# Optimization experiments

Hardware: AMD Instinct MI355X
Metric: run time of the kernel (lower is better)

## Reference

```python
import jax, jax.numpy as jnp
import numpy as np

EMBED = 1024
HEADS = 16
HEAD_SIZE = EMBED // HEADS


def setup_inputs() -> dict:
    key = jax.random.key(0)
    ks = jax.random.split(key, 12)
    B, S = 2, 2048
    s = 1.0 / np.sqrt(EMBED)
    return {
        "querys": jax.random.normal(ks[0], (B, S, EMBED), jnp.float32),
        "keys": jax.random.normal(ks[1], (B, S, EMBED), jnp.float32),
        "values": jax.random.normal(ks[2], (B, S, EMBED), jnp.float32),
        "Wq": jax.random.normal(ks[3], (EMBED, EMBED), jnp.float32) * s,
        "bq": jax.random.normal(ks[4], (EMBED,), jnp.float32) * s,
        "Wk": jax.random.normal(ks[5], (EMBED, EMBED), jnp.float32) * s,
        "bk": jax.random.normal(ks[6], (EMBED,), jnp.float32) * s,
        "Wv": jax.random.normal(ks[7], (EMBED, EMBED), jnp.float32) * s,
        "bv": jax.random.normal(ks[8], (EMBED,), jnp.float32) * s,
        "Wo": jax.random.normal(ks[9], (EMBED, EMBED), jnp.float32) * s,
        "bo": jax.random.normal(ks[10], (EMBED,), jnp.float32) * s,
    }


def reference(querys, keys, values, Wq, bq, Wk, bk, Wv, bv, Wo, bo):
    B, S, E = querys.shape
    H, D = HEADS, HEAD_SIZE
    # torch nn.Linear: y = x @ W.T + b
    q = (querys @ Wq.T + bq).reshape(B, S, H, D).transpose(0, 2, 1, 3)  # [B,H,S,D]
    k = (keys @ Wk.T + bk).reshape(B, S, H, D).transpose(0, 2, 1, 3)
    v = (values @ Wv.T + bv).reshape(B, S, H, D).transpose(0, 2, 1, 3)
    # NOTE: original scales by head_size**0.05 (faithful to source, likely a bug)
    scale = D ** 0.05
    energy = jnp.einsum("bhqd,bhkd->bhqk", q, k) / scale  # [B,H,S,S]
    attention = jax.nn.softmax(energy, axis=-1)
    out = jnp.einsum("bhqk,bhkd->bhqd", attention, v)  # [B,H,S,D]
    out = out.transpose(0, 2, 1, 3).reshape(B, S, E)
    return out @ Wo.T + bo
```

## Files before the change

kernel.cpp:

```cpp
#include <hip/hip_runtime.h>

typedef __attribute__((ext_vector_type(4))) float f32x4;
typedef __attribute__((ext_vector_type(8))) float f32x8;
typedef __attribute__((ext_vector_type(8))) unsigned short ushort8;
typedef __attribute__((ext_vector_type(4))) unsigned short ushort4v;
typedef __attribute__((ext_vector_type(8))) __bf16 bf16x8;

#define QSCALE 1.17183256f

#if __has_builtin(__builtin_amdgcn_exp2f)
#define EXP2(x) __builtin_amdgcn_exp2f(x)
#else
#define EXP2(x) exp2f(x)
#endif

__device__ __forceinline__ unsigned short f2bf(float x) {
  unsigned u = __float_as_uint(x);
  u += 0x7FFFu + ((u >> 16) & 1u);
  return (unsigned short)(u >> 16);
}

__device__ __forceinline__ ushort8 cvt8(const float* src) {
  float4 x0 = *(const float4*)src;
  float4 x1 = *(const float4*)(src + 4);
  ushort8 v;
  v[0] = f2bf(x0.x); v[1] = f2bf(x0.y); v[2] = f2bf(x0.z); v[3] = f2bf(x0.w);
  v[4] = f2bf(x1.x); v[5] = f2bf(x1.y); v[6] = f2bf(x1.z); v[7] = f2bf(x1.w);
  return v;
}

__device__ __forceinline__ f32x4 mfma16(ushort8 a, ushort8 b, f32x4 c) {
  return __builtin_amdgcn_mfma_f32_16x16x32_bf16(
      __builtin_bit_cast(bf16x8, a), __builtin_bit_cast(bf16x8, b), c, 0, 0, 0);
}
__device__ __forceinline__ f32x4 mfma16b(bf16x8 a, ushort8 b, f32x4 c) {
  return __builtin_amdgcn_mfma_f32_16x16x32_bf16(
      a, __builtin_bit_cast(bf16x8, b), c, 0, 0, 0);
}

__device__ __forceinline__ void gload_lds16(const void* g, void* l) {
  __builtin_amdgcn_global_load_lds(
      (const __attribute__((address_space(1))) void*)g,
      (__attribute__((address_space(3))) void*)l, 16, 0, 0);
}

__global__ __launch_bounds__(256) void cvt_f32_bf16(
    const float* __restrict__ s0, const float* __restrict__ s1, const float* __restrict__ s2,
    const float* __restrict__ s3, const float* __restrict__ s4, const float* __restrict__ s5,
    const float* __restrict__ s6, unsigned short* __restrict__ dstA,
    unsigned short* __restrict__ dstW)
{
  const int z = blockIdx.y;
  const float* src;
  unsigned short* dst;
  int n;
  if (z < 3) {
    src = (z == 0) ? s0 : (z == 1) ? s1 : s2;
    dst = dstA + (size_t)z * 4194304;
    n = 4194304;
  } else {
    src = (z == 3) ? s3 : (z == 4) ? s4 : (z == 5) ? s5 : s6;
    dst = dstW + (size_t)(z - 3) * 1048576;
    n = 1048576;
  }
  int i = (blockIdx.x * 256 + threadIdx.x) * 8;
  const int stride = gridDim.x * 256 * 8;
  for (; i < n; i += stride) *(ushort8*)(dst + i) = cvt8(src + i);
}

__global__ __launch_bounds__(256) void gemm_qkv_bf(
    const unsigned short* __restrict__ Abf, const unsigned short* __restrict__ Wbf,
    const float* __restrict__ bq, const float* __restrict__ bk, const float* __restrict__ bv,
    unsigned short* __restrict__ Qb, unsigned short* __restrict__ Kb,
    unsigned short* __restrict__ Vtb)
{
  __shared__ __align__(16) unsigned short Sl[4][4096];
  const int lin = blockIdx.x + 8 * blockIdx.y + 256 * blockIdx.z;
  const int swz = (lin & 7) * 96 + (lin >> 3);
  const int bx = swz & 7, by = (swz >> 3) & 31, z = swz >> 8;

  const unsigned short* Ap = Abf + (size_t)z * 4194304;
  const unsigned short* Wp = Wbf + (size_t)z * 1048576;
  const float* bp = (z == 0) ? bq : (z == 1) ? bk : bv;

  const int t = threadIdx.x, l = t & 63, w = t >> 6;
  const int lr = l & 15, g = l >> 4;
  const int wm = (w >> 1) * 64, wn = (w & 1) * 64;

  int prow[2], pcol[2];
#pragma unroll
  for (int j = 0; j < 2; ++j) {
    int p = j * 256 + w * 64 + l;
    prow[j] = p >> 2;
    pcol[j] = (p & 3) ^ ((prow[j] >> 1) & 3);
  }

  char* lds0 = (char*)&Sl[0][0];
  const int arow0 = wm + lr, brow0 = wn + lr;
  const int abyte = (arow0 * 32 + (g ^ ((arow0 >> 1) & 3)) * 8) * 2;
  const int bbyte = 8192 + (brow0 * 32 + (g ^ ((brow0 >> 1) & 3)) * 8) * 2;

  f32x4 acc[4][4] = {};

#define STAGE_QKV(bufoff, k0)                                                     \
  {                                                                               \
    _Pragma("unroll") for (int j = 0; j < 2; ++j) {                               \
      gload_lds16(Ap + (size_t)(by * 128 + prow[j]) * 1024 + (k0) + pcol[j] * 8,  \
                  lds0 + (bufoff) + (j * 256 + w * 64) * 16);                     \
      gload_lds16(Wp + (size_t)(bx * 128 + prow[j]) * 1024 + (k0) + pcol[j] * 8,  \
                  lds0 + (bufoff) + 8192 + (j * 256 + w * 64) * 16);              \
    }                                                                             \
  }

  STAGE_QKV(0, 0)
  __syncthreads();

  for (int kt = 0; kt < 32; ++kt) {
    const int curoff = (kt & 1) << 14;
    if (kt < 31) STAGE_QKV(curoff ^ 16384, (kt + 1) * 32)
    const char* pa = lds0 + curoff;
    ushort8 a[4], b[4];
#pragma unroll
    for (int m = 0; m < 4; ++m)
      a[m] = *(const ushort8*)(pa + abyte + m * 1024);
#pragma unroll
    for (int n = 0; n < 4; ++n)
      b[n] = *(const ushort8*)(pa + bbyte + n * 1024);
#pragma unroll
    for (int m = 0; m < 4; ++m)
#pragma unroll
      for (int n = 0; n < 4; ++n)
        acc[m][n] = mfma16(a[m], b[n], acc[m][n]);
    __syncthreads();
  }

  float bias_n[4];
#pragma unroll
  for (int n = 0; n < 4; ++n) bias_n[n] = bp[bx * 128 + wn + n * 16 + lr];

  if (z < 2) {
    const float sc = (z == 0) ? QSCALE : 1.0f;
    unsigned short* Cp = z ? Kb : Qb;
#pragma unroll
    for (int m = 0; m < 4; ++m)
#pragma unroll
      for (int n = 0; n < 4; ++n)
#pragma unroll
        for (int r = 0; r < 4; ++r) {
          float v = (acc[m][n][r] + bias_n[n]) * sc;
          int gm = by * 128 + wm + m * 16 + g * 4 + r;
          int gn = bx * 128 + wn + n * 16 + lr;
          int bb = gm >> 11, s = gm & 2047;
          int h = gn >> 6, d = gn & 63;
          Cp[((size_t)((bb * 16 + h) * 2048 + s) << 6) + d] = f2bf(v);
        }
  } else {
#pragma unroll
    for (int m = 0; m < 4; ++m) {
      int gm0 = by * 128 + wm + m * 16 + g * 4;
      int bb = gm0 >> 11, s0 = gm0 & 2047;
#pragma unroll
      for (int n = 0; n < 4; ++n) {
        int gn = bx * 128 + wn + n * 16 + lr;
        int h = gn >> 6, d = gn & 63;
        ushort4v pk;
#pragma unroll
        for (int r = 0; r < 4; ++r) pk[r] = f2bf(acc[m][n][r] + bias_n[n]);
        *(ushort4v*)&Vtb[((size_t)((bb * 16 + h) * 64 + d) << 11) + s0] = pk;
      }
    }
  }
}

__global__ __launch_bounds__(256) void gemm_o_bf(
    const unsigned short* __restrict__ AO, const unsigned short* __restrict__ Wp,
    const float* __restrict__ bo, float* __restrict__ C)
{
  __shared__ __align__(16) unsigned short Al[2][128 * 32];
  __shared__ __align__(16) unsigned short Wl[2][64 * 32];
  const int lin = blockIdx.x + 16 * blockIdx.y;
  const int swz = (lin & 7) * 64 + (lin >> 3);
  const int bx = swz & 15, by = swz >> 4;

  const int t = threadIdx.x, l = t & 63, w = t >> 6;
  const int lr = l & 15, g = l >> 4;
  const int wm = w * 32;

  int prow[2], pcol[2];
#pragma unroll
  for (int j = 0; j < 2; ++j) {
    int p = j * 256 + w * 64 + l;
    prow[j] = p >> 2;
    pcol[j] = (p & 3) ^ ((prow[j] >> 1) & 3);
  }

  f32x4 acc[2][4] = {};

#define STAGE_O(buf, k0)                                                          \
  {                                                                               \
    _Pragma("unroll") for (int j = 0; j < 2; ++j) {                               \
      gload_lds16(AO + (size_t)(by * 128 + prow[j]) * 1024 + (k0) + pcol[j] * 8,  \
                  &Al[buf][(j * 256 + w * 64) * 8]);                              \
    }                                                                             \
    gload_lds16(Wp + (size_t)(bx * 64 + prow[0]) * 1024 + (k0) + pcol[0] * 8,     \
                &Wl[buf][(w * 64) * 8]);                                          \
  }

  STAGE_O(0, 0)
  __syncthreads();

  for (int kt = 0; kt < 32; ++kt) {
    const int cur = kt & 1;
    if (kt < 31) STAGE_O(cur ^ 1, (kt + 1) * 32)
    ushort8 a[2], b[4];
#pragma unroll
    for (int m = 0; m < 2; ++m) {
      int r = wm + m * 16 + lr;
      a[m] = *(const ushort8*)&Al[cur][r * 32 + (g ^ ((r >> 1) & 3)) * 8];
    }
#pragma unroll
    for (int n = 0; n < 4; ++n) {
      int r = n * 16 + lr;
      b[n] = *(const ushort8*)&Wl[cur][r * 32 + (g ^ ((r >> 1) & 3)) * 8];
    }
#pragma unroll
    for (int m = 0; m < 2; ++m)
#pragma unroll
      for (int n = 0; n < 4; ++n)
        acc[m][n] = mfma16(a[m], b[n], acc[m][n]);
    __syncthreads();
  }

  float bias_n[4];
#pragma unroll
  for (int n = 0; n < 4; ++n) bias_n[n] = bo[bx * 64 + n * 16 + lr];

#pragma unroll
  for (int m = 0; m < 2; ++m)
#pragma unroll
    for (int n = 0; n < 4; ++n)
#pragma unroll
      for (int r = 0; r < 4; ++r) {
        int gm = by * 128 + wm + m * 16 + g * 4 + r;
        int gn = bx * 64 + n * 16 + lr;
        C[(size_t)gm * 1024 + gn] = acc[m][n][r] + bias_n[n];
      }
}

__global__ __launch_bounds__(512) void attn_fwd(
    const unsigned short* __restrict__ Qb, const unsigned short* __restrict__ Kb,
    const unsigned short* __restrict__ Vtb, unsigned short* __restrict__ AO)
{
  __shared__ __align__(16) unsigned short Kl[4][64 * 64];
  __shared__ __align__(16) unsigned short Vl[4][64 * 64];
  const int t = threadIdx.x;
  const int l = t & 63, w = t >> 6;
  const int lr = l & 15, g = l >> 4;
  const int wq = w & 3, kh = w >> 2;
  const int lin = blockIdx.x + 16 * blockIdx.y;
  const int swz = (lin & 7) * 64 + (lin >> 3);
  const int qt = swz & 15, bh = swz >> 4;

  const unsigned short* Qh = Qb + (size_t)bh * (2048 * 64);
  const unsigned short* Kh = Kb + (size_t)bh * (2048 * 64);
  const unsigned short* Vth = Vtb + (size_t)bh * (64 * 2048);

  ushort8 aq[2][2];
#pragma unroll
  for (int m = 0; m < 2; ++m)
#pragma unroll
    for (int kk = 0; kk < 2; ++kk) {
      int q = qt * 128 + wq * 32 + m * 16 + lr;
      aq[m][kk] = *(const ushort8*)&Qh[q * 64 + kk * 32 + g * 8];
    }

  ushort8 ones;
#pragma unroll
  for (int j = 0; j < 8; ++j) ones[j] = 0x3F80;

  f32x4 o[2][4] = {};
  f32x4 lacc[2] = {};

  const int sr = t >> 3, sc = t & 7;
  ushort8 rk, rv;

#define STAGE_ATTN(buf)                                                      \
  {                                                                          \
    *(ushort8*)&Kl[buf][sr * 64 + ((sc ^ (sr & 7))) * 8] = rk;               \
    _Pragma("unroll") for (int h = 0; h < 2; ++h) {                          \
      int tw = 2 * sc + h;                                                   \
      int n4 = tw >> 2, gg = tw & 3;                                         \
      int chunk = ((n4 >> 1) << 2) + gg;                                     \
      int within = (n4 & 1) << 2;                                            \
      ushort4v hv = h ? __builtin_shufflevector(rv, rv, 4, 5, 6, 7)          \
                      : __builtin_shufflevector(rv, rv, 0, 1, 2, 3);         \
      *(ushort4v*)&Vl[buf][sr * 64 + ((chunk ^ (sr & 7))) * 8 + within] = hv;\
    }                                                                        \
  }

#define LOAD_NEXT(tile)                                                      \
  {                                                                          \
    rk = *(const ushort8*)&Kh[((tile) * 64 + sr) * 64 + sc * 8];             \
    rv = *(const ushort8*)&Vth[sr * 2048 + (tile) * 64 + sc * 8];            \
  }

#define COMPUTE_ATTN(cur)                                                    \
  {                                                                          \
    f32x4 s[2][2] = {};                                                      \
    __builtin_amdgcn_s_setprio(1);                                           \
    _Pragma("unroll") for (int kk = 0; kk < 2; ++kk) {                       \
      _Pragma("unroll") for (int n = 0; n < 2; ++n) {                        \
        ushort8 ak = *(const ushort8*)&Kl[cur][(kh * 32 + n * 16 + lr) * 64 +\
                                              (((kk * 4 + g) ^ (lr & 7))) * 8]; \
        _Pragma("unroll") for (int m = 0; m < 2; ++m)                        \
          s[n][m] = mfma16(ak, aq[m][kk], s[n][m]);                          \
      }                                                                      \
    }                                                                        \
    __builtin_amdgcn_s_setprio(0);                                           \
    float p[2][2][4];                                                        \
    _Pragma("unroll") for (int n = 0; n < 2; ++n)                            \
      _Pragma("unroll") for (int m = 0; m < 2; ++m)                          \
        _Pragma("unroll") for (int r = 0; r < 4; ++r)                        \
          p[n][m][r] = EXP2(s[n][m][r]);                                     \
    bf16x8 pa[2];                                                            \
    _Pragma("unroll") for (int m = 0; m < 2; ++m) {                          \
      f32x8 v = {p[0][m][0], p[0][m][1], p[0][m][2], p[0][m][3],             \
                 p[1][m][0], p[1][m][1], p[1][m][2], p[1][m][3]};            \
      pa[m] = __builtin_convertvector(v, bf16x8);                            \
    }                                                                        \
    __builtin_amdgcn_s_setprio(1);                                           \
    _Pragma("unroll") for (int m = 0; m < 2; ++m)                            \
      lacc[m] = mfma16b(pa[m], ones, lacc[m]);                               \
    _Pragma("unroll") for (int n = 0; n < 4; ++n) {                          \
      int d = n * 16 + lr;                                                   \
      ushort8 bv = *(const ushort8*)&Vl[cur][d * 64 +                        \
                                            (((kh * 4 + g) ^ (d & 7))) * 8]; \
      _Pragma("unroll") for (int m = 0; m < 2; ++m)                          \
        o[m][n] = mfma16b(pa[m], bv, o[m][n]);                               \
    }                                                                        \
    __builtin_amdgcn_s_setprio(0);                                           \
  }

  LOAD_NEXT(0)
  STAGE_ATTN(0)
  LOAD_NEXT(1)
  STAGE_ATTN(1)
  __syncthreads();

  for (int jj = 0; jj < 8; ++jj) {
    LOAD_NEXT(4 * jj + 2)
    COMPUTE_ATTN(0)
    STAGE_ATTN(2)
    LOAD_NEXT(4 * jj + 3)
    COMPUTE_ATTN(1)
    STAGE_ATTN(3)
    __syncthreads();
    if (jj < 7) LOAD_NEXT(4 * jj + 4)
    COMPUTE_ATTN(2)
    if (jj < 7) STAGE_ATTN(0)
    if (jj < 7) LOAD_NEXT(4 * jj + 5)
    COMPUTE_ATTN(3)
    if (jj < 7) STAGE_ATTN(1)
    __syncthreads();
  }

  __syncthreads();
  float* Of = (float*)&Kl[0][0];
  if (kh == 1) {
#pragma unroll
    for (int m = 0; m < 2; ++m)
#pragma unroll
      for (int n = 0; n < 4; ++n)
#pragma unroll
        for (int r = 0; r < 4; ++r)
          Of[(wq * 32 + m * 16 + g * 4 + r) * 64 + n * 16 + lr] = o[m][n][r];
  }
  __syncthreads();
  if (kh == 0) {
#pragma unroll
    for (int m = 0; m < 2; ++m)
#pragma unroll
      for (int n = 0; n < 4; ++n)
#pragma unroll
        for (int r = 0; r < 4; ++r)
          o[m][n][r] += Of[(wq * 32 + m * 16 + g * 4 + r) * 64 + n * 16 + lr];
  }
  __syncthreads();
  float* Lf = (float*)&Kl[0][0];
  if (kh == 1 && lr == 0) {
#pragma unroll
    for (int m = 0; m < 2; ++m)
#pragma unroll
      for (int r = 0; r < 4; ++r)
        Lf[wq * 32 + m * 16 + g * 4 + r] = lacc[m][r];
  }
  __syncthreads();
  if (kh == 0) {
    const int bb = bh >> 4, h = bh & 15;
#pragma unroll
    for (int m = 0; m < 2; ++m) {
      float inv[4];
#pragma unroll
      for (int r = 0; r < 4; ++r)
        inv[r] = 1.0f / (lacc[m][r] + Lf[wq * 32 + m * 16 + g * 4 + r]);
#pragma unroll
      for (int n = 0; n < 4; ++n)
#pragma unroll
        for (int r = 0; r < 4; ++r) {
          int q = qt * 128 + wq * 32 + m * 16 + g * 4 + r;
          AO[(size_t)(bb * 2048 + q) * 1024 + h * 64 + n * 16 + lr] =
              f2bf(o[m][n][r] * inv[r]);
        }
    }
  }
}

__global__ __launch_bounds__(256) void gemm_qkv_f32(
    const float* __restrict__ Aq, const float* __restrict__ Ak, const float* __restrict__ Av,
    const float* __restrict__ Wq, const float* __restrict__ Wk, const float* __restrict__ Wv,
    const float* __restrict__ bq, const float* __restrict__ bk, const float* __restrict__ bv,
    unsigned short* __restrict__ Qb, unsigned short* __restrict__ Kb, unsigned short* __restrict__ Vtb)
{
  __shared__ __align__(16) unsigned short Al[128 * 32];
  __shared__ __align__(16) unsigned short Wl[128 * 32];
  const int z = blockIdx.z;
  const float* Ap = (z == 0) ? Aq : (z == 1) ? Ak : Av;
  const float* Wp = (z == 0) ? Wq : (z == 1) ? Wk : Wv;
  const float* bp = (z == 0) ? bq : (z == 1) ? bk : bv;

  const int t = threadIdx.x;
  const int l = t & 63, w = t >> 6;
  const int lr = l & 15, g = l >> 4;
  const int wm = (w >> 1) * 64, wn = (w & 1) * 64;
  const int bx = blockIdx.x, by = blockIdx.y;
  const int r0 = t >> 2, c0 = t & 3;

  f32x4 acc[4][4] = {};

  for (int k0 = 0; k0 < 1024; k0 += 32) {
    __syncthreads();
#pragma unroll
    for (int i = 0; i < 2; ++i) {
      int r = r0 + i * 64;
      int cs = c0 ^ ((r >> 1) & 3);
      *(ushort8*)&Al[r * 32 + cs * 8] = cvt8(Ap + (size_t)(by * 128 + r) * 1024 + k0 + c0 * 8);
      *(ushort8*)&Wl[r * 32 + cs * 8] = cvt8(Wp + (size_t)(bx * 128 + r) * 1024 + k0 + c0 * 8);
    }
    __syncthreads();
    ushort8 a[4], b[4];
#pragma unroll
    for (int m = 0; m < 4; ++m) {
      int r = wm + m * 16 + lr;
      a[m] = *(const ushort8*)&Al[r * 32 + (g ^ ((r >> 1) & 3)) * 8];
    }
#pragma unroll
    for (int n = 0; n < 4; ++n) {
      int r = wn + n * 16 + lr;
      b[n] = *(const ushort8*)&Wl[r * 32 + (g ^ ((r >> 1) & 3)) * 8];
    }
#pragma unroll
    for (int m = 0; m < 4; ++m)
#pragma unroll
      for (int n = 0; n < 4; ++n)
        acc[m][n] = mfma16(a[m], b[n], acc[m][n]);
  }

  float bias_n[4];
#pragma unroll
  for (int n = 0; n < 4; ++n) bias_n[n] = bp[bx * 128 + wn + n * 16 + lr];

  if (z < 2) {
    const float sc = (z == 0) ? QSCALE : 1.0f;
    unsigned short* Cp = z ? Kb : Qb;
#pragma unroll
    for (int m = 0; m < 4; ++m)
#pragma unroll
      for (int n = 0; n < 4; ++n)
#pragma unroll
        for (int r = 0; r < 4; ++r) {
          float v = (acc[m][n][r] + bias_n[n]) * sc;
          int gm = by * 128 + wm + m * 16 + g * 4 + r;
          int gn = bx * 128 + wn + n * 16 + lr;
          int bb = gm >> 11, s = gm & 2047;
          int h = gn >> 6, d = gn & 63;
          Cp[((size_t)((bb * 16 + h) * 2048 + s) << 6) + d] = f2bf(v);
        }
  } else {
#pragma unroll
    for (int m = 0; m < 4; ++m) {
      int gm0 = by * 128 + wm + m * 16 + g * 4;
      int bb = gm0 >> 11, s0 = gm0 & 2047;
#pragma unroll
      for (int n = 0; n < 4; ++n) {
        int gn = bx * 128 + wn + n * 16 + lr;
        int h = gn >> 6, d = gn & 63;
        ushort4v pk;
#pragma unroll
        for (int r = 0; r < 4; ++r) pk[r] = f2bf(acc[m][n][r] + bias_n[n]);
        *(ushort4v*)&Vtb[((size_t)((bb * 16 + h) * 64 + d) << 11) + s0] = pk;
      }
    }
  }
}

__global__ __launch_bounds__(256) void gemm_o_f32(
    const unsigned short* __restrict__ AO, const float* __restrict__ Wo,
    const float* __restrict__ bo, float* __restrict__ C)
{
  __shared__ __align__(16) unsigned short Al[128 * 32];
  __shared__ __align__(16) unsigned short Wl[64 * 32];
  const int t = threadIdx.x;
  const int l = t & 63, w = t >> 6;
  const int lr = l & 15, g = l >> 4;
  const int wm = w * 32;
  const int bx = blockIdx.x, by = blockIdx.y;
  const int r0 = t >> 2, c0 = t & 3;

  f32x4 acc[2][4] = {};

  for (int k0 = 0; k0 < 1024; k0 += 32) {
    __syncthreads();
#pragma unroll
    for (int i = 0; i < 2; ++i) {
      int r = r0 + i * 64;
      int cs = c0 ^ ((r >> 1) & 3);
      *(ushort8*)&Al[r * 32 + cs * 8] =
          *(const ushort8*)&AO[(size_t)(by * 128 + r) * 1024 + k0 + c0 * 8];
    }
    {
      int r = r0;
      int cs = c0 ^ ((r >> 1) & 3);
      *(ushort8*)&Wl[r * 32 + cs * 8] = cvt8(Wo + (size_t)(bx * 64 + r) * 1024 + k0 + c0 * 8);
    }
    __syncthreads();
    ushort8 a[2], b[4];
#pragma unroll
    for (int m = 0; m < 2; ++m) {
      int r = wm + m * 16 + lr;
      a[m] = *(const ushort8*)&Al[r * 32 + (g ^ ((r >> 1) & 3)) * 8];
    }
#pragma unroll
    for (int n = 0; n < 4; ++n) {
      int r = n * 16 + lr;
      b[n] = *(const ushort8*)&Wl[r * 32 + (g ^ ((r >> 1) & 3)) * 8];
    }
#pragma unroll
    for (int m = 0; m < 2; ++m)
#pragma unroll
      for (int n = 0; n < 4; ++n)
        acc[m][n] = mfma16(a[m], b[n], acc[m][n]);
  }

  float bias_n[4];
#pragma unroll
  for (int n = 0; n < 4; ++n) bias_n[n] = bo[bx * 64 + n * 16 + lr];

#pragma unroll
  for (int m = 0; m < 2; ++m)
#pragma unroll
    for (int n = 0; n < 4; ++n)
#pragma unroll
      for (int r = 0; r < 4; ++r) {
        int gm = by * 128 + wm + m * 16 + g * 4 + r;
        int gn = bx * 64 + n * 16 + lr;
        C[(size_t)gm * 1024 + gn] = acc[m][n][r] + bias_n[n];
      }
}

extern "C" void kernel_launch(void* const* d_in, const int* in_sizes, int n_in,
                              void* d_out, int out_size, void* d_ws, size_t ws_size,
                              hipStream_t stream) {
  (void)in_sizes; (void)n_in; (void)out_size;
  const float* querys = (const float*)d_in[0];
  const float* keys   = (const float*)d_in[1];
  const float* values = (const float*)d_in[2];
  const float* Wq = (const float*)d_in[3];
  const float* bq = (const float*)d_in[4];
  const float* Wk = (const float*)d_in[5];
  const float* bk = (const float*)d_in[6];
  const float* Wv = (const float*)d_in[7];
  const float* bv = (const float*)d_in[8];
  const float* Wo = (const float*)d_in[9];
  const float* bo = (const float*)d_in[10];

  const size_t need = (size_t)29360128 * 2;
  if (ws_size >= need) {
    unsigned short* Wbf = (unsigned short*)d_ws;
    unsigned short* Qb  = Wbf + 4194304;
    unsigned short* Kb  = Qb + 4194304;
    unsigned short* Vtb = Kb + 4194304;
    unsigned short* Abf = Vtb + 4194304;
    unsigned short* AO  = Abf;

    cvt_f32_bf16<<<dim3(1024, 7), 256, 0, stream>>>(querys, keys, values, Wq, Wk, Wv, Wo,
                                                    Abf, Wbf);
    gemm_qkv_bf<<<dim3(8, 32, 3), 256, 0, stream>>>(Abf, Wbf, bq, bk, bv, Qb, Kb, Vtb);
    attn_fwd<<<dim3(16, 32), 512, 0, stream>>>(Qb, Kb, Vtb, AO);
    gemm_o_bf<<<dim3(16, 32), 256, 0, stream>>>(AO, Wbf + 3 * 1048576, bo, (float*)d_out);
  } else {
    unsigned short* Qb  = (unsigned short*)d_ws;
    unsigned short* Kb  = Qb + (size_t)4194304;
    unsigned short* Vtb = Kb + (size_t)4194304;
    unsigned short* AO  = Vtb + (size_t)4194304;

    gemm_qkv_f32<<<dim3(8, 32, 3), 256, 0, stream>>>(querys, keys, values, Wq, Wk, Wv,
                                                     bq, bk, bv, Qb, Kb, Vtb);
    attn_fwd<<<dim3(16, 32), 512, 0, stream>>>(Qb, Kb, Vtb, AO);
    gemm_o_f32<<<dim3(16, 32), 256, 0, stream>>>(AO, Wo, bo, (float*)d_out);
  }
}
```

Measured before the change: 120.4 us.

## Fuse activation fp32-to-bf16 conversion into QKV GEMM LDS staging

Stops pre-converting the three activation tensors to bf16 in a separate pass. The QKV GEMM now stages fp32 activation tiles straight into LDS with a new XOR swizzle and converts them to bf16 in registers before the MFMA. The weight-only conversion kernel remains. This removes a full write and re-read of 12M bf16 activations, at the cost of double the global and LDS traffic for A tiles inside the GEMM, a larger LDS footprint (48KB), and extra conversion instructions in the inner loop.

```diff
diff --git a/kernel.cpp b/kernel.cpp
--- a/kernel.cpp
+++ b/kernel.cpp
@@ -44,42 +44,31 @@
       (__attribute__((address_space(3))) void*)l, 16, 0, 0);
 }
 
-__global__ __launch_bounds__(256) void cvt_f32_bf16(
-    const float* __restrict__ s0, const float* __restrict__ s1, const float* __restrict__ s2,
+__global__ __launch_bounds__(256) void cvt_w_bf16(
     const float* __restrict__ s3, const float* __restrict__ s4, const float* __restrict__ s5,
-    const float* __restrict__ s6, unsigned short* __restrict__ dstA,
-    unsigned short* __restrict__ dstW)
+    const float* __restrict__ s6, unsigned short* __restrict__ dstW)
 {
   const int z = blockIdx.y;
-  const float* src;
-  unsigned short* dst;
-  int n;
-  if (z < 3) {
-    src = (z == 0) ? s0 : (z == 1) ? s1 : s2;
-    dst = dstA + (size_t)z * 4194304;
-    n = 4194304;
-  } else {
-    src = (z == 3) ? s3 : (z == 4) ? s4 : (z == 5) ? s5 : s6;
-    dst = dstW + (size_t)(z - 3) * 1048576;
-    n = 1048576;
-  }
+  const float* src = (z == 0) ? s3 : (z == 1) ? s4 : (z == 2) ? s5 : s6;
+  unsigned short* dst = dstW + (size_t)z * 1048576;
   int i = (blockIdx.x * 256 + threadIdx.x) * 8;
   const int stride = gridDim.x * 256 * 8;
-  for (; i < n; i += stride) *(ushort8*)(dst + i) = cvt8(src + i);
+  for (; i < 1048576; i += stride) *(ushort8*)(dst + i) = cvt8(src + i);
 }
 
 __global__ __launch_bounds__(256) void gemm_qkv_bf(
-    const unsigned short* __restrict__ Abf, const unsigned short* __restrict__ Wbf,
+    const float* __restrict__ Aq, const float* __restrict__ Ak, const float* __restrict__ Av,
+    const unsigned short* __restrict__ Wbf,
     const float* __restrict__ bq, const float* __restrict__ bk, const float* __restrict__ bv,
     unsigned short* __restrict__ Qb, unsigned short* __restrict__ Kb,
     unsigned short* __restrict__ Vtb)
 {
-  __shared__ __align__(16) unsigned short Sl[4][4096];
+  __shared__ __align__(16) char Sl[49152];
   const int lin = blockIdx.x + 8 * blockIdx.y + 256 * blockIdx.z;
   const int swz = (lin & 7) * 96 + (lin >> 3);
   const int bx = swz & 7, by = (swz >> 3) & 31, z = swz >> 8;
 
-  const unsigned short* Ap = Abf + (size_t)z * 4194304;
+  const float* Af = (z == 0) ? Aq : (z == 1) ? Ak : Av;
   const unsigned short* Wp = Wbf + (size_t)z * 1048576;
   const float* bp = (z == 0) ? bq : (z == 1) ? bk : bv;
 
@@ -87,50 +76,66 @@
   const int lr = l & 15, g = l >> 4;
   const int wm = (w >> 1) * 64, wn = (w & 1) * 64;
 
-  int prow[2], pcol[2];
+  int aprow[4], apch[4];
+#pragma unroll
+  for (int j = 0; j < 4; ++j) {
+    int p = j * 256 + t;
+    aprow[j] = p >> 3;
+    apch[j] = (p & 7) ^ (aprow[j] & 7);
+  }
+  int wprow[2], wpcol[2];
 #pragma unroll
   for (int j = 0; j < 2; ++j) {
-    int p = j * 256 + w * 64 + l;
-    prow[j] = p >> 2;
-    pcol[j] = (p & 3) ^ ((prow[j] >> 1) & 3);
-  }
-
-  char* lds0 = (char*)&Sl[0][0];
-  const int arow0 = wm + lr, brow0 = wn + lr;
-  const int abyte = (arow0 * 32 + (g ^ ((arow0 >> 1) & 3)) * 8) * 2;
-  const int bbyte = 8192 + (brow0 * 32 + (g ^ ((brow0 >> 1) & 3)) * 8) * 2;
+    int p = j * 256 + t;
+    wprow[j] = p >> 2;
+    wpcol[j] = (p & 3) ^ ((wprow[j] >> 1) & 3);
+  }
+
+  char* lds0 = &Sl[0];
+  const int abase = (wm + lr) * 128;
+  const int aoff0 = abase + (((2 * g) ^ (lr & 7)) << 4);
+  const int aoff1 = abase + (((2 * g + 1) ^ (lr & 7)) << 4);
+  const int brow0 = wn + lr;
+  const int bbyte = (brow0 * 32 + (g ^ ((brow0 >> 1) & 3)) * 8) * 2;
 
   f32x4 acc[4][4] = {};
 
-#define STAGE_QKV(bufoff, k0)                                                     \
+#define STAGE_QKV(aoffb, woffb, k0)                                               \
   {                                                                               \
-    _Pragma("unroll") for (int j = 0; j < 2; ++j) {                               \
-      gload_lds16(Ap + (size_t)(by * 128 + prow[j]) * 1024 + (k0) + pcol[j] * 8,  \
-                  lds0 + (bufoff) + (j * 256 + w * 64) * 16);                     \
-      gload_lds16(Wp + (size_t)(bx * 128 + prow[j]) * 1024 + (k0) + pcol[j] * 8,  \
-                  lds0 + (bufoff) + 8192 + (j * 256 + w * 64) * 16);              \
-    }                                                                             \
-  }
-
-  STAGE_QKV(0, 0)
+    _Pragma("unroll") for (int j = 0; j < 4; ++j)                                 \
+      gload_lds16(Af + (size_t)(by * 128 + aprow[j]) * 1024 + (k0) + apch[j] * 4, \
+                  lds0 + (aoffb) + (j * 256 + w * 64) * 16);                      \
+    _Pragma("unroll") for (int j = 0; j < 2; ++j)                                 \
+      gload_lds16(Wp + (size_t)(bx * 128 + wprow[j]) * 1024 + (k0) + wpcol[j] * 8,\
+                  lds0 + (woffb) + (j * 256 + w * 64) * 16);                      \
+  }
+
+  STAGE_QKV(0, 32768, 0)
   __syncthreads();
 
   for (int kt = 0; kt < 32; ++kt) {
-    const int curoff = (kt & 1) << 14;
-    if (kt < 31) STAGE_QKV(curoff ^ 16384, (kt + 1) * 32)
-    const char* pa = lds0 + curoff;
-    ushort8 a[4], b[4];
+    const int aoffc = (kt & 1) << 14;
+    const int woffc = 32768 + ((kt & 1) << 13);
+    if (kt < 31) STAGE_QKV(aoffc ^ 16384, woffc ^ 8192, (kt + 1) * 32)
+    const char* pa = lds0 + aoffc;
+    const char* pw = lds0 + woffc;
+    bf16x8 af[4];
+    ushort8 b[4];
+#pragma unroll
+    for (int m = 0; m < 4; ++m) {
+      f32x4 lo = *(const f32x4*)(pa + aoff0 + m * 2048);
+      f32x4 hi = *(const f32x4*)(pa + aoff1 + m * 2048);
+      f32x8 v = {lo[0], lo[1], lo[2], lo[3], hi[0], hi[1], hi[2], hi[3]};
+      af[m] = __builtin_convertvector(v, bf16x8);
+    }
+#pragma unroll
+    for (int n = 0; n < 4; ++n)
+      b[n] = *(const ushort8*)(pw + bbyte + n * 1024);
 #pragma unroll
     for (int m = 0; m < 4; ++m)
-      a[m] = *(const ushort8*)(pa + abyte + m * 1024);
-#pragma unroll
-    for (int n = 0; n < 4; ++n)
-      b[n] = *(const ushort8*)(pa + bbyte + n * 1024);
-#pragma unroll
-    for (int m = 0; m < 4; ++m)
-#pragma unroll
-      for (int n = 0; n < 4; ++n)
-        acc[m][n] = mfma16(a[m], b[n], acc[m][n]);
+#pragma unroll
+      for (int n = 0; n < 4; ++n)
+        acc[m][n] = mfma16b(af[m], b[n], acc[m][n]);
     __syncthreads();
   }
 
@@ -589,12 +594,11 @@
     unsigned short* Qb  = Wbf + 4194304;
     unsigned short* Kb  = Qb + 4194304;
     unsigned short* Vtb = Kb + 4194304;
-    unsigned short* Abf = Vtb + 4194304;
-    unsigned short* AO  = Abf;
-
-    cvt_f32_bf16<<<dim3(1024, 7), 256, 0, stream>>>(querys, keys, values, Wq, Wk, Wv, Wo,
-                                                    Abf, Wbf);
-    gemm_qkv_bf<<<dim3(8, 32, 3), 256, 0, stream>>>(Abf, Wbf, bq, bk, bv, Qb, Kb, Vtb);
+    unsigned short* AO  = Vtb + 4194304;
+
+    cvt_w_bf16<<<dim3(512, 4), 256, 0, stream>>>(Wq, Wk, Wv, Wo, Wbf);
+    gemm_qkv_bf<<<dim3(8, 32, 3), 256, 0, stream>>>(querys, keys, values, Wbf,
+                                                    bq, bk, bv, Qb, Kb, Vtb);
     attn_fwd<<<dim3(16, 32), 512, 0, stream>>>(Qb, Kb, Vtb, AO);
     gemm_o_bf<<<dim3(16, 32), 256, 0, stream>>>(AO, Wbf + 3 * 1048576, bo, (float*)d_out);
   } else {
```

New measurement: 121.5 us. No clear change (+0.9%).
